# Optimization experiments

Hardware: AMD Instinct MI355X
Metric: run time of the kernel (lower is better)

The kernel has to match this reference:

```python
import jax, jax.numpy as jnp
import numpy as np

NUM_TABLES = 26
VOCAB = 100000
D = 128          # sparse_feature_size == mlp_bot[-1]
B = 8192
P = 10           # fixed pooling factor per bag
DENSE = 13
BOT = [512, 256, 128]
TOP = [1024, 1024, 512, 256, 1]
NF = NUM_TABLES + 1  # features entering dot interaction


def setup_inputs() -> dict:
    key = jax.random.key(0)
    ks = iter(jax.random.split(key, 32))
    inp = {}
    inp["dense_x"] = jax.random.normal(next(ks), (B, DENSE), dtype=jnp.float32)
    inp["sparse_indices"] = jax.random.randint(next(ks), (NUM_TABLES, B * P), 0, VOCAB, dtype=jnp.int32)
    # EmbeddingBag weights init: uniform(-0.01, 0.01)
    inp["emb_tables"] = jax.random.uniform(next(ks), (NUM_TABLES, VOCAB, D), jnp.float32, -0.01, 0.01)
    def xavier(k, shape):
        fan_out, fan_in = shape
        lim = np.sqrt(6.0 / (fan_in + fan_out)).astype(np.float32)
        return jax.random.uniform(k, shape, jnp.float32, -lim, lim)
    dims_bot = [DENSE] + BOT
    for i in range(len(BOT)):
        inp[f"bot_w{i}"] = xavier(next(ks), (dims_bot[i + 1], dims_bot[i]))
        inp[f"bot_b{i}"] = jnp.zeros((dims_bot[i + 1],), jnp.float32)
    interact_dim = NF * (NF - 1) // 2 + BOT[-1]  # 351 + 128 = 479
    dims_top = [interact_dim] + TOP
    for i in range(len(TOP)):
        inp[f"top_w{i}"] = xavier(next(ks), (dims_top[i + 1], dims_top[i]))
        inp[f"top_b{i}"] = jnp.zeros((dims_top[i + 1],), jnp.float32)
    return inp


def reference(dense_x, sparse_indices, emb_tables,
              bot_w0, bot_b0, bot_w1, bot_b1, bot_w2, bot_b2,
              top_w0, top_b0, top_w1, top_b1, top_w2, top_b2,
              top_w3, top_b3, top_w4, top_b4):
    # bottom MLP (Linear + ReLU on every layer)
    x = dense_x
    for w, b in ((bot_w0, bot_b0), (bot_w1, bot_b1), (bot_w2, bot_b2)):
        x = jax.nn.relu(x @ w.T + b)  # [B, 128]

    # multi-table EmbeddingBag sum pooling (fixed pooling factor P)
    idx = sparse_indices.reshape(NUM_TABLES, B, P)
    ly = jax.vmap(lambda tab, i: tab[i].sum(axis=1))(emb_tables, idx)  # [T, B, D]

    # dot interaction: bmm + upper-triangular gather
    T_feat = jnp.concatenate([x[None], ly], axis=0).transpose(1, 0, 2)  # [B, NF, D]
    Z = jnp.einsum('bnd,bmd->bnm', T_feat, T_feat)                       # [B, NF, NF]
    li, lj = np.triu_indices(NF, k=1)
    Zflat = Z[:, li, lj]                                                 # [B, NF*(NF-1)/2]
    z = jnp.concatenate([x, Zflat], axis=1)                              # [B, 479]

    # top MLP: ReLU on all but last layer
    h = z
    tops = ((top_w0, top_b0), (top_w1, top_b1), (top_w2, top_b2), (top_w3, top_b3))
    for w, b in tops:
        h = jax.nn.relu(h @ w.T + b)
    p = h @ top_w4.T + top_b4  # [B, 1]
    return jax.nn.sigmoid(p.squeeze(1))
```

## Files before the change

### kernel.cpp

```cpp
#include <hip/hip_runtime.h>
#include <hip/hip_bf16.h>
#include <cstdint>

typedef __attribute__((ext_vector_type(8))) short bf16x8;
typedef __attribute__((ext_vector_type(4))) float f32x4;

#define B_SZ 8192
#define NF 27
#define TROW 3456

__device__ __forceinline__ void gld_lds16(const void* g, void* l) {
    __builtin_amdgcn_global_load_lds(
        (const __attribute__((address_space(1))) unsigned int*)g,
        (__attribute__((address_space(3))) unsigned int*)l, 16, 0, 0);
}

struct CvtJob { const float* in; __hip_bfloat16* out; int N, K, Kp; };
struct CvtJobs { CvtJob j[8]; int start[9]; };

__global__ __launch_bounds__(256) void cvt_all(CvtJobs jobs) {
    int gid = blockIdx.x * 256 + threadIdx.x;
    if (gid >= jobs.start[8]) return;
    int k = 0;
    #pragma unroll
    for (int i = 1; i < 8; i++) if (gid >= jobs.start[i]) k = i;
    const CvtJob& J = jobs.j[k];
    int local = gid - jobs.start[k];
    int n = local / J.Kp, kk = local - n * J.Kp;
    float v = (kk < J.K) ? J.in[(size_t)n * J.K + kk] : 0.f;
    J.out[local] = __float2bfloat16(v);
}

__global__ __launch_bounds__(256) void emb_kernel(const int* __restrict__ idx,
                                                  const float* __restrict__ tab,
                                                  __hip_bfloat16* __restrict__ T) {
    int lane = threadIdx.x & 63, wv = threadIdx.x >> 6;
    int p = blockIdx.x * 4 + wv;
    int t = p >> 13;
    int b = p & 8191;
    const int* ip = idx + (size_t)t * 81920 + b * 10;
    const float* tb = tab + (size_t)t * 100000 * 128;
    float ax = 0.f, ay = 0.f;
    #pragma unroll
    for (int j = 0; j < 10; j++) {
        int r = ip[j];
        const float2* src = (const float2*)(tb + (size_t)r * 128) + lane;
        float2 v = *src;
        ax += v.x; ay += v.y;
    }
    __hip_bfloat162 o;
    o.x = __float2bfloat16(ax);
    o.y = __float2bfloat16(ay);
    ((__hip_bfloat162*)(T + (size_t)b * TROW + (1 + t) * 128))[lane] = o;
}

template<int TM, int TN, int WM, int WN, int RELU>
__global__ __launch_bounds__(256) void gemm_t(const __hip_bfloat16* __restrict__ A,
                                              const __hip_bfloat16* __restrict__ W,
                                              const float* __restrict__ bias,
                                              __hip_bfloat16* __restrict__ C,
                                              int M, int N, int K, int ldc) {
    constexpr int ROWS = TM + TN;
    constexpr int CH = ROWS * 4 / 256;
    constexpr int MI = TM / WM / 16;
    constexpr int NI = TN / WN / 16;
    __shared__ __align__(16) __hip_bfloat16 ABs[ROWS * 32];

    const int tid = threadIdx.x;
    const int lane = tid & 63, wave = tid >> 6;
    const int wmI = wave / WN, wnI = wave % WN;
    const int m0 = blockIdx.y * TM, n0 = blockIdx.x * TN;

    const __hip_bfloat16* gp[CH];
    #pragma unroll
    for (int c = 0; c < CH; c++) {
        int gid = c * 256 + tid;
        int row = gid >> 2, col = (gid & 3) * 8;
        gp[c] = (row < TM ? A + (size_t)(m0 + row) * K
                          : W + (size_t)(n0 + row - TM) * K) + col;
    }

    f32x4 acc[MI][NI] = {};
    const int fr = lane & 15, fkb = (lane >> 4) * 8;

    for (int k0 = 0; k0 < K; k0 += 32) {
        __syncthreads();
        #pragma unroll
        for (int c = 0; c < CH; c++)
            gld_lds16(gp[c] + k0, &ABs[(c * 256 + wave * 64) * 8]);
        asm volatile("s_waitcnt vmcnt(0)" ::: "memory");
        __syncthreads();
        bf16x8 a[MI], b[NI];
        #pragma unroll
        for (int i = 0; i < MI; i++)
            a[i] = *(const bf16x8*)&ABs[(wmI * (TM / WM) + i * 16 + fr) * 32 + fkb];
        #pragma unroll
        for (int j = 0; j < NI; j++)
            b[j] = *(const bf16x8*)&ABs[(TM + wnI * (TN / WN) + j * 16 + fr) * 32 + fkb];
        #pragma unroll
        for (int i = 0; i < MI; i++)
            #pragma unroll
            for (int j = 0; j < NI; j++)
                acc[i][j] = __builtin_amdgcn_mfma_f32_16x16x32_bf16(a[i], b[j], acc[i][j], 0, 0, 0);
    }

    const int fq = lane >> 4;
    #pragma unroll
    for (int i = 0; i < MI; i++) {
        #pragma unroll
        for (int j = 0; j < NI; j++) {
            int n = n0 + wnI * (TN / WN) + j * 16 + fr;
            float bv = bias[n];
            #pragma unroll
            for (int r = 0; r < 4; r++) {
                int m = m0 + wmI * (TM / WM) + i * 16 + fq * 4 + r;
                float v = acc[i][j][r] + bv;
                if (RELU) v = fmaxf(v, 0.f);
                C[(size_t)m * ldc + n] = __float2bfloat16(v);
            }
        }
    }
}

__global__ __launch_bounds__(256) void interact_kernel(const __hip_bfloat16* __restrict__ T,
                                                       __hip_bfloat16* __restrict__ z) {
    __shared__ __align__(16) __hip_bfloat16 S[4][32 * 128];
    int lane = threadIdx.x & 63, wave = threadIdx.x >> 6;
    int b = blockIdx.x * 4 + wave;
    __hip_bfloat16* Sw = S[wave];
    const uint4* src = (const uint4*)(T + (size_t)b * TROW);
    uint4* dst = (uint4*)Sw;
    for (int i = lane; i < 432; i += 64) dst[i] = src[i];
    uint4 z4 = {0u, 0u, 0u, 0u};
    for (int i = 432 + lane; i < 512; i += 64) dst[i] = z4;
    __syncthreads();

    const int fr = lane & 15, fkb = (lane >> 4) * 8;
    bf16x8 fr2[2][4];
    #pragma unroll
    for (int mi = 0; mi < 2; mi++)
        #pragma unroll
        for (int kt = 0; kt < 4; kt++)
            fr2[mi][kt] = *(const bf16x8*)&Sw[(mi * 16 + fr) * 128 + kt * 32 + fkb];

    f32x4 acc[2][2] = {};
    #pragma unroll
    for (int kt = 0; kt < 4; kt++)
        #pragma unroll
        for (int mi = 0; mi < 2; mi++)
            #pragma unroll
            for (int ni = 0; ni < 2; ni++)
                acc[mi][ni] = __builtin_amdgcn_mfma_f32_16x16x32_bf16(fr2[mi][kt], fr2[ni][kt], acc[mi][ni], 0, 0, 0);

    __hip_bfloat16* zb = z + (size_t)b * 512;
    zb[lane] = Sw[lane];
    zb[64 + lane] = Sw[64 + lane];
    if (lane < 33) zb[479 + lane] = __float2bfloat16(0.f);
    const int fq = lane >> 4;
    #pragma unroll
    for (int mi = 0; mi < 2; mi++) {
        #pragma unroll
        for (int ni = 0; ni < 2; ni++) {
            #pragma unroll
            for (int r = 0; r < 4; r++) {
                int m = mi * 16 + fq * 4 + r;
                int n = ni * 16 + fr;
                if (m < 27 && n < 27 && m < n) {
                    int p = m * 26 - (m * (m - 1)) / 2 + (n - m - 1);
                    zb[128 + p] = __float2bfloat16(acc[mi][ni][r]);
                }
            }
        }
    }
}

__global__ __launch_bounds__(256) void final_kernel(const __hip_bfloat16* __restrict__ h,
                                                    const float* __restrict__ w,
                                                    const float* __restrict__ bias,
                                                    float* __restrict__ out) {
    int lane = threadIdx.x & 63, wv = threadIdx.x >> 6;
    int s = blockIdx.x * 4 + wv;
    const __hip_bfloat16* hp = h + (size_t)s * 256;
    float sum = 0.f;
    #pragma unroll
    for (int i = 0; i < 4; i++) {
        int k = i * 64 + lane;
        sum += __bfloat162float(hp[k]) * w[k];
    }
    #pragma unroll
    for (int off = 32; off; off >>= 1) sum += __shfl_down(sum, off, 64);
    if (lane == 0) out[s] = 1.f / (1.f + expf(-(sum + bias[0])));
}

extern "C" void kernel_launch(void* const* d_in, const int* in_sizes, int n_in,
                              void* d_out, int out_size, void* d_ws, size_t ws_size,
                              hipStream_t stream) {
    const float* dense_x = (const float*)d_in[0];
    const int* sidx      = (const int*)d_in[1];
    const float* emb     = (const float*)d_in[2];
    const float* bw0 = (const float*)d_in[3];  const float* bb0 = (const float*)d_in[4];
    const float* bw1 = (const float*)d_in[5];  const float* bb1 = (const float*)d_in[6];
    const float* bw2 = (const float*)d_in[7];  const float* bb2 = (const float*)d_in[8];
    const float* tw0 = (const float*)d_in[9];  const float* tb0 = (const float*)d_in[10];
    const float* tw1 = (const float*)d_in[11]; const float* tb1 = (const float*)d_in[12];
    const float* tw2 = (const float*)d_in[13]; const float* tb2 = (const float*)d_in[14];
    const float* tw3 = (const float*)d_in[15]; const float* tb3 = (const float*)d_in[16];
    const float* tw4 = (const float*)d_in[17]; const float* tb4 = (const float*)d_in[18];
    float* out = (float*)d_out;

    char* ws = (char*)d_ws;
    size_t off = 0;
    auto alloc = [&](size_t bytes) {
        off = (off + 255) & ~(size_t)255;
        void* p = ws + off;
        off += bytes;
        return p;
    };
    __hip_bfloat16* A0  = (__hip_bfloat16*)alloc((size_t)B_SZ * 32 * 2);
    __hip_bfloat16* Wb0 = (__hip_bfloat16*)alloc((size_t)512 * 32 * 2);
    __hip_bfloat16* Wb1 = (__hip_bfloat16*)alloc((size_t)256 * 512 * 2);
    __hip_bfloat16* Wb2 = (__hip_bfloat16*)alloc((size_t)128 * 256 * 2);
    __hip_bfloat16* Wt0 = (__hip_bfloat16*)alloc((size_t)1024 * 512 * 2);
    __hip_bfloat16* Wt1 = (__hip_bfloat16*)alloc((size_t)1024 * 1024 * 2);
    __hip_bfloat16* Wt2 = (__hip_bfloat16*)alloc((size_t)512 * 1024 * 2);
    __hip_bfloat16* Wt3 = (__hip_bfloat16*)alloc((size_t)256 * 512 * 2);
    __hip_bfloat16* bufA = (__hip_bfloat16*)alloc((size_t)B_SZ * 1024 * 2);
    __hip_bfloat16* bufB = (__hip_bfloat16*)alloc((size_t)B_SZ * 1024 * 2);
    __hip_bfloat16* Tbuf = (__hip_bfloat16*)alloc((size_t)B_SZ * TROW * 2);
    __hip_bfloat16* zbuf = (__hip_bfloat16*)alloc((size_t)B_SZ * 512 * 2);

    CvtJobs cj;
    auto setJob = [&](int i, const float* in, __hip_bfloat16* o, int N, int K, int Kp) {
        cj.j[i] = {in, o, N, K, Kp};
    };
    setJob(0, dense_x, A0, B_SZ, 13, 32);
    setJob(1, bw0, Wb0, 512, 13, 32);
    setJob(2, bw1, Wb1, 256, 512, 512);
    setJob(3, bw2, Wb2, 128, 256, 256);
    setJob(4, tw0, Wt0, 1024, 479, 512);
    setJob(5, tw1, Wt1, 1024, 1024, 1024);
    setJob(6, tw2, Wt2, 512, 1024, 1024);
    setJob(7, tw3, Wt3, 256, 512, 512);
    cj.start[0] = 0;
    for (int i = 0; i < 8; i++) cj.start[i + 1] = cj.start[i] + cj.j[i].N * cj.j[i].Kp;
    int totalCvt = cj.start[8];
    cvt_all<<<(totalCvt + 255) / 256, 256, 0, stream>>>(cj);

    gemm_t<128,128,2,2,1><<<dim3(512/128, B_SZ/128), 256, 0, stream>>>(A0, Wb0, bb0, bufA, B_SZ, 512, 32, 512);
    gemm_t<128, 64,2,2,1><<<dim3(256/ 64, B_SZ/128), 256, 0, stream>>>(bufA, Wb1, bb1, bufB, B_SZ, 256, 512, 256);
    gemm_t< 64, 64,2,2,1><<<dim3(128/ 64, B_SZ/ 64), 256, 0, stream>>>(bufB, Wb2, bb2, Tbuf, B_SZ, 128, 256, TROW);

    emb_kernel<<<26 * B_SZ / 4, 256, 0, stream>>>(sidx, emb, Tbuf);

    interact_kernel<<<B_SZ / 4, 256, 0, stream>>>(Tbuf, zbuf);

    gemm_t<128,128,2,2,1><<<dim3(1024/128, B_SZ/128), 256, 0, stream>>>(zbuf, Wt0, tb0, bufA, B_SZ, 1024, 512, 1024);
    gemm_t<128,128,2,2,1><<<dim3(1024/128, B_SZ/128), 256, 0, stream>>>(bufA, Wt1, tb1, bufB, B_SZ, 1024, 1024, 1024);
    gemm_t<128, 64,2,2,1><<<dim3( 512/ 64, B_SZ/128), 256, 0, stream>>>(bufB, Wt2, tb2, bufA, B_SZ, 512, 1024, 512);
    gemm_t<128, 64,2,2,1><<<dim3( 256/ 64, B_SZ/128), 256, 0, stream>>>(bufA, Wt3, tb3, bufB, B_SZ, 256, 512, 256);

    final_kernel<<<B_SZ / 4, 256, 0, stream>>>(bufB, tw4, tb4, out);
}
```

Baseline: 337.4 us.

## Fuse stages into role-dispatched kernels and pipeline batch quarters across layers

Replaces the per-stage kernel launches with a single role-dispatched kernel launched several times. Each launch co-schedules blocks from different stages on different batch slices, for example embedding gathers of later quarters alongside bottom-MLP GEMMs, or top-MLP layers on a tail slice alongside the next layer of the main slice. The goal is to hide the memory-bound embedding gather behind compute and to fill the GPU during small-grid layers. It also computes the first bottom layer (K=13) directly in fp32 instead of converting and padding, and drops the dense-input conversion. The cost is a single 128x128 tile configuration for all GEMMs, a larger shared-memory footprint for every block, and tight cross-slice dependencies that must be respected by launch order.

```diff
diff --git a/kernel.cpp b/kernel.cpp
--- a/kernel.cpp
+++ b/kernel.cpp
@@ -6,7 +6,7 @@
 typedef __attribute__((ext_vector_type(4))) float f32x4;
 
 #define B_SZ 8192
-#define NF 27
+#define QS 2048
 #define TROW 3456
 
 __device__ __forceinline__ void gld_lds16(const void* g, void* l) {
@@ -15,37 +15,91 @@
         (__attribute__((address_space(3))) unsigned int*)l, 16, 0, 0);
 }
 
+#define RT_GEMM 0
+#define RT_EMB  1
+#define RT_INT  2
+#define RT_FIN  3
+#define RT_CVT  4
+#define RT_B0   5
+
+struct Role { int type, i0, i1, i2; const void *a, *b, *c; void *d; };
+struct Sched { Role r[3]; int start[3]; int nr; };
 struct CvtJob { const float* in; __hip_bfloat16* out; int N, K, Kp; };
-struct CvtJobs { CvtJob j[8]; int start[9]; };
-
-__global__ __launch_bounds__(256) void cvt_all(CvtJobs jobs) {
-    int gid = blockIdx.x * 256 + threadIdx.x;
-    if (gid >= jobs.start[8]) return;
-    int k = 0;
-    #pragma unroll
-    for (int i = 1; i < 8; i++) if (gid >= jobs.start[i]) k = i;
-    const CvtJob& J = jobs.j[k];
-    int local = gid - jobs.start[k];
-    int n = local / J.Kp, kk = local - n * J.Kp;
-    float v = (kk < J.K) ? J.in[(size_t)n * J.K + kk] : 0.f;
-    J.out[local] = __float2bfloat16(v);
-}
-
-__global__ __launch_bounds__(256) void emb_kernel(const int* __restrict__ idx,
-                                                  const float* __restrict__ tab,
-                                                  __hip_bfloat16* __restrict__ T) {
-    int lane = threadIdx.x & 63, wv = threadIdx.x >> 6;
-    int p = blockIdx.x * 4 + wv;
-    int t = p >> 13;
-    int b = p & 8191;
+struct CvtJobs { CvtJob j[6]; int start[7]; };
+
+__device__ __forceinline__ void gemm128_dev(int lb, int tid,
+    const __hip_bfloat16* __restrict__ A, const __hip_bfloat16* __restrict__ W,
+    const float* __restrict__ bias, __hip_bfloat16* __restrict__ C,
+    int N, int K, int ldc, char* smem_) {
+    __hip_bfloat16* ABs = (__hip_bfloat16*)smem_;
+    const int lane = tid & 63, wave = tid >> 6;
+    const int wmI = wave >> 1, wnI = wave & 1;
+    const int nbx = N >> 7;
+    const int by = lb / nbx, bx = lb - by * nbx;
+    const int m0 = by * 128, n0 = bx * 128;
+
+    const __hip_bfloat16* gp[4];
+    #pragma unroll
+    for (int c = 0; c < 4; c++) {
+        int gid = c * 256 + tid;
+        int row = gid >> 2, col = (gid & 3) * 8;
+        gp[c] = (row < 128 ? A + (size_t)(m0 + row) * K
+                           : W + (size_t)(n0 + row - 128) * K) + col;
+    }
+
+    f32x4 acc[4][4] = {};
+    const int fr = lane & 15, fkb = (lane >> 4) * 8;
+
+    for (int k0 = 0; k0 < K; k0 += 32) {
+        __syncthreads();
+        #pragma unroll
+        for (int c = 0; c < 4; c++)
+            gld_lds16(gp[c] + k0, &ABs[(c * 256 + wave * 64) * 8]);
+        asm volatile("s_waitcnt vmcnt(0)" ::: "memory");
+        __syncthreads();
+        bf16x8 a[4], b[4];
+        #pragma unroll
+        for (int i = 0; i < 4; i++)
+            a[i] = *(const bf16x8*)&ABs[(wmI * 64 + i * 16 + fr) * 32 + fkb];
+        #pragma unroll
+        for (int j = 0; j < 4; j++)
+            b[j] = *(const bf16x8*)&ABs[(128 + wnI * 64 + j * 16 + fr) * 32 + fkb];
+        #pragma unroll
+        for (int i = 0; i < 4; i++)
+            #pragma unroll
+            for (int j = 0; j < 4; j++)
+                acc[i][j] = __builtin_amdgcn_mfma_f32_16x16x32_bf16(a[i], b[j], acc[i][j], 0, 0, 0);
+    }
+
+    const int fq = lane >> 4;
+    #pragma unroll
+    for (int i = 0; i < 4; i++)
+        #pragma unroll
+        for (int j = 0; j < 4; j++) {
+            int n = n0 + wnI * 64 + j * 16 + fr;
+            float bv = bias[n];
+            #pragma unroll
+            for (int r = 0; r < 4; r++) {
+                int m = m0 + wmI * 64 + i * 16 + fq * 4 + r;
+                C[(size_t)m * ldc + n] = __float2bfloat16(fmaxf(acc[i][j][r] + bv, 0.f));
+            }
+        }
+}
+
+__device__ __forceinline__ void emb_dev(int lb, int tid, int q0,
+    const int* __restrict__ idx, const float* __restrict__ tab,
+    __hip_bfloat16* __restrict__ T) {
+    int lane = tid & 63, wv = tid >> 6;
+    int p = lb * 4 + wv;
+    int t = p >> 11;
+    int b = q0 + (p & (QS - 1));
     const int* ip = idx + (size_t)t * 81920 + b * 10;
     const float* tb = tab + (size_t)t * 100000 * 128;
     float ax = 0.f, ay = 0.f;
     #pragma unroll
     for (int j = 0; j < 10; j++) {
         int r = ip[j];
-        const float2* src = (const float2*)(tb + (size_t)r * 128) + lane;
-        float2 v = *src;
+        float2 v = ((const float2*)(tb + (size_t)r * 128))[lane];
         ax += v.x; ay += v.y;
     }
     __hip_bfloat162 o;
@@ -54,80 +108,11 @@
     ((__hip_bfloat162*)(T + (size_t)b * TROW + (1 + t) * 128))[lane] = o;
 }
 
-template<int TM, int TN, int WM, int WN, int RELU>
-__global__ __launch_bounds__(256) void gemm_t(const __hip_bfloat16* __restrict__ A,
-                                              const __hip_bfloat16* __restrict__ W,
-                                              const float* __restrict__ bias,
-                                              __hip_bfloat16* __restrict__ C,
-                                              int M, int N, int K, int ldc) {
-    constexpr int ROWS = TM + TN;
-    constexpr int CH = ROWS * 4 / 256;
-    constexpr int MI = TM / WM / 16;
-    constexpr int NI = TN / WN / 16;
-    __shared__ __align__(16) __hip_bfloat16 ABs[ROWS * 32];
-
-    const int tid = threadIdx.x;
-    const int lane = tid & 63, wave = tid >> 6;
-    const int wmI = wave / WN, wnI = wave % WN;
-    const int m0 = blockIdx.y * TM, n0 = blockIdx.x * TN;
-
-    const __hip_bfloat16* gp[CH];
-    #pragma unroll
-    for (int c = 0; c < CH; c++) {
-        int gid = c * 256 + tid;
-        int row = gid >> 2, col = (gid & 3) * 8;
-        gp[c] = (row < TM ? A + (size_t)(m0 + row) * K
-                          : W + (size_t)(n0 + row - TM) * K) + col;
-    }
-
-    f32x4 acc[MI][NI] = {};
-    const int fr = lane & 15, fkb = (lane >> 4) * 8;
-
-    for (int k0 = 0; k0 < K; k0 += 32) {
-        __syncthreads();
-        #pragma unroll
-        for (int c = 0; c < CH; c++)
-            gld_lds16(gp[c] + k0, &ABs[(c * 256 + wave * 64) * 8]);
-        asm volatile("s_waitcnt vmcnt(0)" ::: "memory");
-        __syncthreads();
-        bf16x8 a[MI], b[NI];
-        #pragma unroll
-        for (int i = 0; i < MI; i++)
-            a[i] = *(const bf16x8*)&ABs[(wmI * (TM / WM) + i * 16 + fr) * 32 + fkb];
-        #pragma unroll
-        for (int j = 0; j < NI; j++)
-            b[j] = *(const bf16x8*)&ABs[(TM + wnI * (TN / WN) + j * 16 + fr) * 32 + fkb];
-        #pragma unroll
-        for (int i = 0; i < MI; i++)
-            #pragma unroll
-            for (int j = 0; j < NI; j++)
-                acc[i][j] = __builtin_amdgcn_mfma_f32_16x16x32_bf16(a[i], b[j], acc[i][j], 0, 0, 0);
-    }
-
-    const int fq = lane >> 4;
-    #pragma unroll
-    for (int i = 0; i < MI; i++) {
-        #pragma unroll
-        for (int j = 0; j < NI; j++) {
-            int n = n0 + wnI * (TN / WN) + j * 16 + fr;
-            float bv = bias[n];
-            #pragma unroll
-            for (int r = 0; r < 4; r++) {
-                int m = m0 + wmI * (TM / WM) + i * 16 + fq * 4 + r;
-                float v = acc[i][j][r] + bv;
-                if (RELU) v = fmaxf(v, 0.f);
-                C[(size_t)m * ldc + n] = __float2bfloat16(v);
-            }
-        }
-    }
-}
-
-__global__ __launch_bounds__(256) void interact_kernel(const __hip_bfloat16* __restrict__ T,
-                                                       __hip_bfloat16* __restrict__ z) {
-    __shared__ __align__(16) __hip_bfloat16 S[4][32 * 128];
-    int lane = threadIdx.x & 63, wave = threadIdx.x >> 6;
-    int b = blockIdx.x * 4 + wave;
-    __hip_bfloat16* Sw = S[wave];
+__device__ __forceinline__ void interact_dev(int lb, int tid, int q0,
+    const __hip_bfloat16* __restrict__ T, __hip_bfloat16* __restrict__ z, char* smem_) {
+    int lane = tid & 63, wave = tid >> 6;
+    int b = q0 + lb * 4 + wave;
+    __hip_bfloat16* Sw = (__hip_bfloat16*)(smem_ + wave * 8192);
     const uint4* src = (const uint4*)(T + (size_t)b * TROW);
     uint4* dst = (uint4*)Sw;
     for (int i = lane; i < 432; i += 64) dst[i] = src[i];
@@ -158,9 +143,9 @@
     if (lane < 33) zb[479 + lane] = __float2bfloat16(0.f);
     const int fq = lane >> 4;
     #pragma unroll
-    for (int mi = 0; mi < 2; mi++) {
-        #pragma unroll
-        for (int ni = 0; ni < 2; ni++) {
+    for (int mi = 0; mi < 2; mi++)
+        #pragma unroll
+        for (int ni = 0; ni < 2; ni++)
             #pragma unroll
             for (int r = 0; r < 4; r++) {
                 int m = mi * 16 + fq * 4 + r;
@@ -170,16 +155,13 @@
                     zb[128 + p] = __float2bfloat16(acc[mi][ni][r]);
                 }
             }
-        }
-    }
-}
-
-__global__ __launch_bounds__(256) void final_kernel(const __hip_bfloat16* __restrict__ h,
-                                                    const float* __restrict__ w,
-                                                    const float* __restrict__ bias,
-                                                    float* __restrict__ out) {
-    int lane = threadIdx.x & 63, wv = threadIdx.x >> 6;
-    int s = blockIdx.x * 4 + wv;
+}
+
+__device__ __forceinline__ void final_dev(int lb, int tid, int q0,
+    const __hip_bfloat16* __restrict__ h, const float* __restrict__ w,
+    const float* __restrict__ bias, float* __restrict__ out_) {
+    int lane = tid & 63, wv = tid >> 6;
+    int s = q0 + lb * 4 + wv;
     const __hip_bfloat16* hp = h + (size_t)s * 256;
     float sum = 0.f;
     #pragma unroll
@@ -189,7 +171,74 @@
     }
     #pragma unroll
     for (int off = 32; off; off >>= 1) sum += __shfl_down(sum, off, 64);
-    if (lane == 0) out[s] = 1.f / (1.f + expf(-(sum + bias[0])));
+    if (lane == 0) out_[s] = 1.f / (1.f + expf(-(sum + bias[0])));
+}
+
+__device__ __forceinline__ void cvt_dev(int lb, int tid, const CvtJobs& J) {
+    int gid = lb * 256 + tid;
+    if (gid >= J.start[6]) return;
+    int k = 0;
+    #pragma unroll
+    for (int i = 1; i < 6; i++) if (gid >= J.start[i]) k = i;
+    const CvtJob& job = J.j[k];
+    int local = gid - J.start[k];
+    int n = local / job.Kp, kk = local - n * job.Kp;
+    float v = (kk < job.K) ? job.in[(size_t)n * job.K + kk] : 0.f;
+    job.out[local] = __float2bfloat16(v);
+}
+
+__device__ __forceinline__ void bot0_dev(int lb, int tid, const float* __restrict__ x,
+    const float* __restrict__ w, const float* __restrict__ bias,
+    __hip_bfloat16* __restrict__ o, char* smem_) {
+    float* xs = (float*)smem_;
+    int m0 = lb * 4;
+    if (tid < 52) xs[tid] = x[(size_t)m0 * 13 + tid];
+    __syncthreads();
+    for (int c = tid; c < 512; c += 256) {
+        const float* wr = w + (size_t)c * 13;
+        float bv = bias[c];
+        #pragma unroll
+        for (int r = 0; r < 4; r++) {
+            float s = bv;
+            #pragma unroll
+            for (int k = 0; k < 13; k++) s += xs[r * 13 + k] * wr[k];
+            o[(size_t)(m0 + r) * 512 + c] = __float2bfloat16(fmaxf(s, 0.f));
+        }
+    }
+}
+
+__global__ __launch_bounds__(256) void fused_kernel(Sched S, CvtJobs J) {
+    __shared__ __align__(16) char smem[32768];
+    int blk = blockIdx.x;
+    int ri = 0;
+    if (S.nr > 1 && blk >= S.start[1]) ri = 1;
+    if (S.nr > 2 && blk >= S.start[2]) ri = 2;
+    const Role& R = S.r[ri];
+    int lb = blk - S.start[ri];
+    int tid = threadIdx.x;
+    switch (R.type) {
+        case RT_GEMM:
+            gemm128_dev(lb, tid, (const __hip_bfloat16*)R.a, (const __hip_bfloat16*)R.b,
+                        (const float*)R.c, (__hip_bfloat16*)R.d, R.i0, R.i1, R.i2, smem);
+            break;
+        case RT_EMB:
+            emb_dev(lb, tid, R.i0, (const int*)R.a, (const float*)R.b, (__hip_bfloat16*)R.d);
+            break;
+        case RT_INT:
+            interact_dev(lb, tid, R.i0, (const __hip_bfloat16*)R.a, (__hip_bfloat16*)R.d, smem);
+            break;
+        case RT_FIN:
+            final_dev(lb, tid, R.i0, (const __hip_bfloat16*)R.a, (const float*)R.b,
+                      (const float*)R.c, (float*)R.d);
+            break;
+        case RT_CVT:
+            cvt_dev(lb, tid, J);
+            break;
+        case RT_B0:
+            bot0_dev(lb, tid, (const float*)R.a, (const float*)R.b, (const float*)R.c,
+                     (__hip_bfloat16*)R.d, smem);
+            break;
+    }
 }
 
 extern "C" void kernel_launch(void* const* d_in, const int* in_sizes, int n_in,
@@ -216,48 +265,79 @@
         off += bytes;
         return p;
     };
-    __hip_bfloat16* A0  = (__hip_bfloat16*)alloc((size_t)B_SZ * 32 * 2);
-    __hip_bfloat16* Wb0 = (__hip_bfloat16*)alloc((size_t)512 * 32 * 2);
     __hip_bfloat16* Wb1 = (__hip_bfloat16*)alloc((size_t)256 * 512 * 2);
     __hip_bfloat16* Wb2 = (__hip_bfloat16*)alloc((size_t)128 * 256 * 2);
     __hip_bfloat16* Wt0 = (__hip_bfloat16*)alloc((size_t)1024 * 512 * 2);
     __hip_bfloat16* Wt1 = (__hip_bfloat16*)alloc((size_t)1024 * 1024 * 2);
     __hip_bfloat16* Wt2 = (__hip_bfloat16*)alloc((size_t)512 * 1024 * 2);
     __hip_bfloat16* Wt3 = (__hip_bfloat16*)alloc((size_t)256 * 512 * 2);
-    __hip_bfloat16* bufA = (__hip_bfloat16*)alloc((size_t)B_SZ * 1024 * 2);
-    __hip_bfloat16* bufB = (__hip_bfloat16*)alloc((size_t)B_SZ * 1024 * 2);
+    __hip_bfloat16* bufA = (__hip_bfloat16*)alloc((size_t)B_SZ * 512 * 2);
+    __hip_bfloat16* bufB = (__hip_bfloat16*)alloc((size_t)B_SZ * 256 * 2);
     __hip_bfloat16* Tbuf = (__hip_bfloat16*)alloc((size_t)B_SZ * TROW * 2);
     __hip_bfloat16* zbuf = (__hip_bfloat16*)alloc((size_t)B_SZ * 512 * 2);
-
-    CvtJobs cj;
+    __hip_bfloat16* h0   = (__hip_bfloat16*)alloc((size_t)B_SZ * 1024 * 2);
+    __hip_bfloat16* h1   = (__hip_bfloat16*)alloc((size_t)B_SZ * 1024 * 2);
+    __hip_bfloat16* h2   = (__hip_bfloat16*)alloc((size_t)B_SZ * 512 * 2);
+    __hip_bfloat16* h3   = (__hip_bfloat16*)alloc((size_t)B_SZ * 256 * 2);
+
+    CvtJobs J;
     auto setJob = [&](int i, const float* in, __hip_bfloat16* o, int N, int K, int Kp) {
-        cj.j[i] = {in, o, N, K, Kp};
+        J.j[i] = {in, o, N, K, Kp};
     };
-    setJob(0, dense_x, A0, B_SZ, 13, 32);
-    setJob(1, bw0, Wb0, 512, 13, 32);
-    setJob(2, bw1, Wb1, 256, 512, 512);
-    setJob(3, bw2, Wb2, 128, 256, 256);
-    setJob(4, tw0, Wt0, 1024, 479, 512);
-    setJob(5, tw1, Wt1, 1024, 1024, 1024);
-    setJob(6, tw2, Wt2, 512, 1024, 1024);
-    setJob(7, tw3, Wt3, 256, 512, 512);
-    cj.start[0] = 0;
-    for (int i = 0; i < 8; i++) cj.start[i + 1] = cj.start[i] + cj.j[i].N * cj.j[i].Kp;
-    int totalCvt = cj.start[8];
-    cvt_all<<<(totalCvt + 255) / 256, 256, 0, stream>>>(cj);
-
-    gemm_t<128,128,2,2,1><<<dim3(512/128, B_SZ/128), 256, 0, stream>>>(A0, Wb0, bb0, bufA, B_SZ, 512, 32, 512);
-    gemm_t<128, 64,2,2,1><<<dim3(256/ 64, B_SZ/128), 256, 0, stream>>>(bufA, Wb1, bb1, bufB, B_SZ, 256, 512, 256);
-    gemm_t< 64, 64,2,2,1><<<dim3(128/ 64, B_SZ/ 64), 256, 0, stream>>>(bufB, Wb2, bb2, Tbuf, B_SZ, 128, 256, TROW);
-
-    emb_kernel<<<26 * B_SZ / 4, 256, 0, stream>>>(sidx, emb, Tbuf);
-
-    interact_kernel<<<B_SZ / 4, 256, 0, stream>>>(Tbuf, zbuf);
-
-    gemm_t<128,128,2,2,1><<<dim3(1024/128, B_SZ/128), 256, 0, stream>>>(zbuf, Wt0, tb0, bufA, B_SZ, 1024, 512, 1024);
-    gemm_t<128,128,2,2,1><<<dim3(1024/128, B_SZ/128), 256, 0, stream>>>(bufA, Wt1, tb1, bufB, B_SZ, 1024, 1024, 1024);
-    gemm_t<128, 64,2,2,1><<<dim3( 512/ 64, B_SZ/128), 256, 0, stream>>>(bufB, Wt2, tb2, bufA, B_SZ, 512, 1024, 512);
-    gemm_t<128, 64,2,2,1><<<dim3( 256/ 64, B_SZ/128), 256, 0, stream>>>(bufA, Wt3, tb3, bufB, B_SZ, 256, 512, 256);
-
-    final_kernel<<<B_SZ / 4, 256, 0, stream>>>(bufB, tw4, tb4, out);
-}
+    setJob(0, bw1, Wb1, 256, 512, 512);
+    setJob(1, bw2, Wb2, 128, 256, 256);
+    setJob(2, tw0, Wt0, 1024, 479, 512);
+    setJob(3, tw1, Wt1, 1024, 1024, 1024);
+    setJob(4, tw2, Wt2, 512, 1024, 1024);
+    setJob(5, tw3, Wt3, 256, 512, 512);
+    J.start[0] = 0;
+    for (int i = 0; i < 6; i++) J.start[i + 1] = J.start[i] + J.j[i].N * J.j[i].Kp;
+    const int cvtBlocks = (J.start[6] + 255) / 256;
+    const int EMB_BLK = 26 * QS / 4;
+
+    Sched S{};
+    int nr = 0, tot = 0;
+    auto add = [&](int type, int nblk, const void* a, const void* b, const void* c, void* d,
+                   int i0, int i1, int i2) {
+        S.r[nr] = {type, i0, i1, i2, a, b, c, d};
+        S.start[nr] = tot;
+        tot += nblk;
+        nr++;
+    };
+    auto fire = [&]() {
+        S.nr = nr;
+        fused_kernel<<<tot, 256, 0, stream>>>(S, J);
+        S = Sched{}; nr = 0; tot = 0;
+    };
+
+    add(RT_B0, B_SZ / 4, dense_x, bw0, bb0, bufA, 0, 0, 0);
+    add(RT_CVT, cvtBlocks, nullptr, nullptr, nullptr, nullptr, 0, 0, 0);
+    add(RT_EMB, EMB_BLK, sidx, emb, nullptr, Tbuf, 0, 0, 0);
+    fire();
+    add(RT_GEMM, (B_SZ / 128) * (256 / 128), bufA, Wb1, bb1, bufB, 256, 512, 256);
+    add(RT_EMB, EMB_BLK, sidx, emb, nullptr, Tbuf, QS, 0, 0);
+    fire();
+    add(RT_GEMM, (B_SZ / 128) * (128 / 128), bufB, Wb2, bb2, Tbuf, 128, 256, TROW);
+    add(RT_EMB, EMB_BLK, sidx, emb, nullptr, Tbuf, 2 * QS, 0, 0);
+    fire();
+    add(RT_INT, 3 * QS / 4, Tbuf, nullptr, nullptr, zbuf, 0, 0, 0);
+    add(RT_EMB, EMB_BLK, sidx, emb, nullptr, Tbuf, 3 * QS, 0, 0);
+    fire();
+    add(RT_GEMM, 48 * 8, zbuf, Wt0, tb0, h0, 1024, 512, 1024);
+    add(RT_INT, QS / 4, Tbuf, nullptr, nullptr, zbuf, 3 * QS, 0, 0);
+    fire();
+    add(RT_GEMM, 48 * 8, h0, Wt1, tb1, h1, 1024, 1024, 1024);
+    add(RT_GEMM, 16 * 8, zbuf + (size_t)6144 * 512, Wt0, tb0, h0 + (size_t)6144 * 1024, 1024, 512, 1024);
+    fire();
+    add(RT_GEMM, 48 * 4, h1, Wt2, tb2, h2, 512, 1024, 512);
+    add(RT_GEMM, 16 * 8, h0 + (size_t)6144 * 1024, Wt1, tb1, h1 + (size_t)6144 * 1024, 1024, 1024, 1024);
+    fire();
+    add(RT_GEMM, 48 * 2, h2, Wt3, tb3, h3, 256, 512, 256);
+    add(RT_GEMM, 16 * 4, h1 + (size_t)6144 * 1024, Wt2, tb2, h2 + (size_t)6144 * 512, 512, 1024, 512);
+    fire();
+    add(RT_FIN, 3 * QS / 4, h3, tw4, tb4, out, 0, 0, 0);
+    add(RT_GEMM, 16 * 2, h2 + (size_t)6144 * 512, Wt3, tb3, h3 + (size_t)6144 * 256, 256, 512, 256);
+    fire();
+    add(RT_FIN, QS / 4, h3, tw4, tb4, out, 3 * QS, 0, 0);
+    fire();
+}
```

Measured after the change: 409.1 us. 21.3% more time.
